# Kernel tuning notes

Measured on AMD Instinct MI355X. Metric: run time of the kernel, lower is better.

The kernel has to match this reference:

```python
import jax, jax.numpy as jnp
import numpy as np

B, T, V = 16, 512, 10000
E, H = 300, 256


def setup_inputs() -> dict:
    key = jax.random.key(0)
    ks = jax.random.split(key, 6)
    return {
        "input": jax.random.normal(ks[0], (B, T, V), dtype=jnp.float32),
        "hidden": jax.random.normal(ks[1], (B, H), dtype=jnp.float32),
        "W_emb": jax.random.normal(ks[2], (E, V), dtype=jnp.float32) * 0.02,
        "W_w": jax.random.normal(ks[3], (H, E), dtype=jnp.float32) * 0.05,
        "W_u": jax.random.normal(ks[4], (H, H), dtype=jnp.float32) * 0.05,
        "W_v": jax.random.normal(ks[5], (V, H), dtype=jnp.float32) * 0.05,
    }


def reference(input, hidden, W_emb, W_w, W_u, W_v):
    # Elman-style cell WITHOUT nonlinearity on the hidden state (matches source):
    #   e = x_t @ W_emb^T ; h = e @ W_w^T + h_prev @ W_u^T ; out = softmax(h @ W_v^T)
    def step(h, x_t):  # x_t: [B, V], h: [B, H]
        e = x_t @ W_emb.T                      # [B, E]
        h_new = e @ W_w.T + h @ W_u.T          # [B, H]
        out = jax.nn.softmax(h_new @ W_v.T, axis=1)  # [B, V]
        return h_new, out

    xs = jnp.swapaxes(input, 0, 1)             # [T, B, V]
    _, outs = jax.lax.scan(step, hidden, xs)   # outs: [T, B, V]
    return jnp.swapaxes(outs, 0, 1)            # [B, T, V]
```

## Files before the change

### kernel.cpp

```cpp
#include <hip/hip_runtime.h>

typedef __bf16 bf16x8 __attribute__((ext_vector_type(8)));
typedef float f32x4 __attribute__((ext_vector_type(4)));
typedef unsigned short u16x8 __attribute__((ext_vector_type(8)));

#define VP 10016

__device__ __forceinline__ unsigned short f2bf(float x){
  unsigned u = __builtin_bit_cast(unsigned, x);
  u += 0x7fffu + ((u>>16)&1u);
  return (unsigned short)(u>>16);
}
__device__ __forceinline__ float bf2f(unsigned short h){
  unsigned u = ((unsigned)h)<<16;
  return __builtin_bit_cast(float, u);
}

__global__ __launch_bounds__(256) void k_wvf(const float* __restrict__ W_v,
                                             unsigned short* __restrict__ Wvf,
                                             const float* __restrict__ W_u,
                                             unsigned short* __restrict__ Wu_bf){
  if(blockIdx.x >= 160){
    int i = (blockIdx.x-160)*256 + threadIdx.x;
    const float4 v = *(const float4*)(W_u + (size_t)i*4);
    unsigned a = (unsigned)f2bf(v.x) | ((unsigned)f2bf(v.y)<<16);
    unsigned b = (unsigned)f2bf(v.z) | ((unsigned)f2bf(v.w)<<16);
    *(uint2*)(Wu_bf + (size_t)i*4) = make_uint2(a,b);
    return;
  }
  const int t = threadIdx.x;
  const int w = t>>6, lane = t&63;
  const int l15 = lane&15, sl = lane>>4;
  const int vg = blockIdx.x*4 + w;
  const int v = vg*16 + l15;
  #pragma unroll
  for(int kk=0;kk<8;kk++){
    u16x8 pk = {0,0,0,0,0,0,0,0};
    if(v < 10000){
      const float* p = W_v + (size_t)v*256 + kk*32 + sl*8;
      float4 v0 = *(const float4*)p;
      float4 v1 = *(const float4*)(p+4);
      pk[0]=f2bf(v0.x); pk[1]=f2bf(v0.y); pk[2]=f2bf(v0.z); pk[3]=f2bf(v0.w);
      pk[4]=f2bf(v1.x); pk[5]=f2bf(v1.y); pk[6]=f2bf(v1.z); pk[7]=f2bf(v1.w);
    }
    *(u16x8*)(Wvf + ((size_t)vg*8 + kk)*512 + lane*8) = pk;
  }
}

__global__ __launch_bounds__(256) void k_m1(const float* __restrict__ W_w,
                                            const float* __restrict__ W_emb,
                                            unsigned short* __restrict__ M1f){
  __shared__ float4 ww4[16][75];
  const int t = threadIdx.x;
  const int ngrp = blockIdx.y;
  const int n0 = ngrp*16;
  for(int i=t; i<16*75; i+=256){
    int n = i/75, c = i - n*75;
    ww4[n][c] = *(const float4*)(W_w + (size_t)(n0+n)*300 + c*4);
  }
  __syncthreads();
  const int v0 = blockIdx.x*512 + t*2;
  if(v0 >= VP) return;
  const int c  = v0>>5;
  const int sl = (v0>>3)&3;
  const int j  = v0&7;
  unsigned short* outp = M1f + (size_t)(ngrp*313 + c)*512 + sl*128 + j;
  if(v0 >= 10000){
    #pragma unroll
    for(int nn=0;nn<16;nn++) *(unsigned*)&outp[nn*8] = 0u;
    return;
  }
  float acc[16][2];
  #pragma unroll
  for(int nn=0;nn<16;nn++){ acc[nn][0]=0.f; acc[nn][1]=0.f; }
  #pragma unroll 2
  for(int cc=0;cc<75;cc++){
    const float* eb = W_emb + (size_t)(4*cc)*10000 + v0;
    float2 wv0 = *(const float2*)(eb);
    float2 wv1 = *(const float2*)(eb + 10000);
    float2 wv2 = *(const float2*)(eb + 20000);
    float2 wv3 = *(const float2*)(eb + 30000);
    #pragma unroll
    for(int nn=0;nn<16;nn++){
      float4 w = ww4[nn][cc];
      acc[nn][0] += w.x*wv0.x + w.y*wv1.x + w.z*wv2.x + w.w*wv3.x;
      acc[nn][1] += w.x*wv0.y + w.y*wv1.y + w.z*wv2.y + w.w*wv3.y;
    }
  }
  #pragma unroll
  for(int nn=0;nn<16;nn++){
    unsigned pk = (unsigned)f2bf(acc[nn][0]) | ((unsigned)f2bf(acc[nn][1])<<16);
    *(unsigned*)&outp[nn*8] = pk;
  }
}

__global__ __launch_bounds__(512, 4) void k_gemm_a(const float* __restrict__ x,
    const unsigned short* __restrict__ M1f, float* __restrict__ gp, int nsplit){
  __shared__ unsigned short As[32768];
  char* Ab = (char*)As;
  const int t = threadIdx.x;
  const int w = t>>6, lane = t&63;
  const int l15 = lane&15, sl = lane>>4;
  const int mh = w>>2, nq = w&3;
  const int r0 = blockIdx.x*128;
  const int kh = blockIdx.y;
  const int base = 313/nsplit, rem = 313%nsplit;
  const int c0 = kh*base + (kh<rem ? kh : rem);
  const int c1 = c0 + base + (kh<rem ? 1 : 0);

  const unsigned short* mbp[4];
  #pragma unroll
  for(int nt=0;nt<4;nt++)
    mbp[nt] = M1f + (size_t)(nq*4+nt)*313*512 + lane*8;

  f32x4 acc[4][4] = {};
  for(int cs=c0; cs<c1; cs+=8){
    const int cs_n = (c1-cs) < 8 ? (c1-cs) : 8;
    if(lane*4 < cs_n*32){
      const int kk = cs*32 + lane*4;
      const bool ok = (kk + 4 <= 10000);
      const int unit0 = lane>>1;
      const int half8 = (lane&1)*8;
      const float* xp = x + (size_t)(r0 + w*16)*10000 + kk;
      #pragma unroll
      for(int g=0; g<2; g++){
        float4 rX[8];
        #pragma unroll
        for(int j=0;j<8;j++)
          rX[j] = ok ? *(const float4*)(xp + (size_t)(g*8+j)*10000)
                     : float4{0.f,0.f,0.f,0.f};
        #pragma unroll
        for(int j=0;j<8;j++){
          const int r = w*16 + g*8 + j;
          unsigned lo = (unsigned)f2bf(rX[j].x) | ((unsigned)f2bf(rX[j].y)<<16);
          unsigned hi = (unsigned)f2bf(rX[j].z) | ((unsigned)f2bf(rX[j].w)<<16);
          *(uint2*)(Ab + r*512 + (((lane>>1) ^ (r&7))<<4) + half8) = make_uint2(lo,hi);
        }
      }
      (void)unit0;
    }
    __syncthreads();
    for(int cc=0; cc<cs_n; cc++){
      const int c = cs + cc;
      bf16x8 b[4];
      #pragma unroll
      for(int nt=0;nt<4;nt++)
        b[nt] = *(const bf16x8*)(mbp[nt] + (size_t)c*512);
      bf16x8 a[4];
      #pragma unroll
      for(int mt=0;mt<4;mt++){
        const int r = mh*64 + mt*16 + l15;
        const int p = (cc*4 + sl) ^ (l15&7);
        a[mt] = *(const bf16x8*)(Ab + r*512 + p*16);
      }
      #pragma unroll
      for(int mt=0;mt<4;mt++)
        #pragma unroll
        for(int nt=0;nt<4;nt++)
          acc[mt][nt] = __builtin_amdgcn_mfma_f32_16x16x32_bf16(a[mt], b[nt], acc[mt][nt], 0,0,0);
    }
    __syncthreads();
  }

  float* gout = gp + (size_t)kh*2097152;
  #pragma unroll
  for(int mt=0;mt<4;mt++)
    #pragma unroll
    for(int nt=0;nt<4;nt++)
      #pragma unroll
      for(int i2=0;i2<4;i2++){
        int row = r0 + mh*64 + mt*16 + sl*4 + i2;
        int col = nq*64 + nt*16 + l15;
        gout[(size_t)row*256 + col] = acc[mt][nt][i2];
      }
}

__global__ __launch_bounds__(256) void k_reduce(float* __restrict__ gp, int nsplit){
  size_t i = ((size_t)blockIdx.x*256 + threadIdx.x)*4;
  float4 acc = *(const float4*)(gp + i);
  for(int s=1;s<nsplit;s++){
    const float4 v = *(const float4*)(gp + (size_t)s*2097152 + i);
    acc.x+=v.x; acc.y+=v.y; acc.z+=v.z; acc.w+=v.w;
  }
  *(float4*)(gp + i) = acc;
}

__global__ __launch_bounds__(256) void k_matsq(const float* __restrict__ A,
    const float* __restrict__ B, float* __restrict__ C){
  int i = blockIdx.x, j = threadIdx.x;
  __shared__ float arow[256];
  arow[j] = A[i*256 + j];
  __syncthreads();
  float acc = 0.f;
  for(int k=0;k<256;k++) acc += arow[k]*B[k*256 + j];
  C[i*256 + j] = acc;
}

__global__ __launch_bounds__(256) void k_scan_local(const float* __restrict__ g,
    const unsigned short* __restrict__ Wu, float* __restrict__ u_final){
  __shared__ unsigned short ub[2][16*256];
  const int m = blockIdx.x;
  const int t = threadIdx.x, wave=t>>6, lane=t&63, l15=lane&15, sl=lane>>4;
  for(int i=t;i<2048;i+=256) ((unsigned*)ub[0])[i] = 0u;
  __syncthreads();
  int buf = 0;
  for(int j=0;j<16;j++){
    float gv[4][4];
    #pragma unroll
    for(int nt=0;nt<4;nt++)
      #pragma unroll
      for(int i=0;i<4;i++){
        int b = sl*4 + i;
        int n = wave*64 + nt*16 + l15;
        size_t r = (size_t)b*512 + m*16 + j;
        gv[nt][i] = g[r*256 + n];
      }
    bf16x8 af[8];
    #pragma unroll
    for(int kk=0;kk<8;kk++){
      int slot = kk*4 + sl;
      af[kk] = *(const bf16x8*)&ub[buf][l15*256 + ((slot ^ (l15&7))<<3)];
    }
    f32x4 acc[4] = {};
    #pragma unroll
    for(int kk=0;kk<8;kk++)
      #pragma unroll
      for(int nt=0;nt<4;nt++){
        int n = wave*64 + nt*16 + l15;
        bf16x8 bv = *(const bf16x8*)&Wu[(size_t)n*256 + kk*32 + sl*8];
        acc[nt] = __builtin_amdgcn_mfma_f32_16x16x32_bf16(af[kk], bv, acc[nt], 0,0,0);
      }
    #pragma unroll
    for(int nt=0;nt<4;nt++)
      #pragma unroll
      for(int i=0;i<4;i++){
        int b = sl*4 + i;
        int n = wave*64 + nt*16 + l15;
        float v = acc[nt][i] + gv[nt][i];
        ub[buf^1][b*256 + (((n>>3) ^ (b&7))<<3) + (n&7)] = f2bf(v);
        if(j==15) u_final[m*4096 + b*256 + n] = v;
      }
    __syncthreads();
    buf ^= 1;
  }
}

__global__ __launch_bounds__(1024) void k_chunk_scan(const float* __restrict__ hidden,
    const float* __restrict__ u_final, const float* __restrict__ A16,
    float* __restrict__ h_start){
  const int b = blockIdx.x;
  const int t = threadIdx.x;
  const int n = t & 255, q = t >> 8;
  __shared__ float hc[256];
  __shared__ float part[3][256];
  float a[64];
  const float* ap = A16 + (size_t)n*256 + q*64;
  #pragma unroll
  for(int i=0;i<16;i++){
    float4 v = *(const float4*)(ap + i*4);
    a[i*4]=v.x; a[i*4+1]=v.y; a[i*4+2]=v.z; a[i*4+3]=v.w;
  }
  if(q==0){
    float h = hidden[b*256 + n];
    hc[n] = h;
    h_start[b*256 + n] = h;
  }
  __syncthreads();
  for(int m=1;m<32;m++){
    float acc0=0.f, acc1=0.f;
    #pragma unroll
    for(int i=0;i<64;i+=2){
      acc0 += a[i]  *hc[q*64 + i];
      acc1 += a[i+1]*hc[q*64 + i+1];
    }
    float acc = acc0 + acc1;
    if(q) part[q-1][n] = acc;
    __syncthreads();
    if(q==0){
      float v = acc + part[0][n] + part[1][n] + part[2][n]
              + u_final[(size_t)(m-1)*4096 + b*256 + n];
      hc[n] = v;
      h_start[(size_t)m*4096 + b*256 + n] = v;
    }
    __syncthreads();
  }
}

__global__ __launch_bounds__(256) void k_scan_fix(const float* __restrict__ g,
    const unsigned short* __restrict__ Wu, const float* __restrict__ h_start,
    unsigned short* __restrict__ h_bf){
  __shared__ unsigned short ub[2][16*256];
  const int m = blockIdx.x;
  const int t=threadIdx.x, wave=t>>6, lane=t&63, l15=lane&15, sl=lane>>4;
  for(int u=t; u<512; u+=256){
    int b = u>>5, s = u&31;
    const float* hp = h_start + m*4096 + b*256 + s*8;
    float4 v0 = *(const float4*)hp;
    float4 v1 = *(const float4*)(hp+4);
    u16x8 pk;
    pk[0]=f2bf(v0.x); pk[1]=f2bf(v0.y); pk[2]=f2bf(v0.z); pk[3]=f2bf(v0.w);
    pk[4]=f2bf(v1.x); pk[5]=f2bf(v1.y); pk[6]=f2bf(v1.z); pk[7]=f2bf(v1.w);
    *(u16x8*)&ub[0][b*256 + ((s ^ (b&7))<<3)] = pk;
  }
  __syncthreads();
  int buf = 0;
  for(int j=0;j<16;j++){
    float gv[4][4];
    #pragma unroll
    for(int nt=0;nt<4;nt++)
      #pragma unroll
      for(int i=0;i<4;i++){
        int b = sl*4 + i;
        int n = wave*64 + nt*16 + l15;
        size_t r = (size_t)b*512 + m*16 + j;
        gv[nt][i] = g[r*256 + n];
      }
    bf16x8 af[8];
    #pragma unroll
    for(int kk=0;kk<8;kk++){
      int slot = kk*4 + sl;
      af[kk] = *(const bf16x8*)&ub[buf][l15*256 + ((slot ^ (l15&7))<<3)];
    }
    f32x4 acc[4] = {};
    #pragma unroll
    for(int kk=0;kk<8;kk++)
      #pragma unroll
      for(int nt=0;nt<4;nt++){
        int n = wave*64 + nt*16 + l15;
        bf16x8 bv = *(const bf16x8*)&Wu[(size_t)n*256 + kk*32 + sl*8];
        acc[nt] = __builtin_amdgcn_mfma_f32_16x16x32_bf16(af[kk], bv, acc[nt], 0,0,0);
      }
    #pragma unroll
    for(int nt=0;nt<4;nt++)
      #pragma unroll
      for(int i=0;i<4;i++){
        int b = sl*4 + i;
        int n = wave*64 + nt*16 + l15;
        float v = acc[nt][i] + gv[nt][i];
        unsigned short hb = f2bf(v);
        ub[buf^1][b*256 + (((n>>3) ^ (b&7))<<3) + (n&7)] = hb;
        size_t r = (size_t)b*512 + m*16 + j;
        h_bf[r*256 + n] = hb;
      }
    __syncthreads();
    buf ^= 1;
  }
}

__global__ __launch_bounds__(512, 4) void k_gemm_c(const unsigned short* __restrict__ h_bf,
    const unsigned short* __restrict__ Wvf, char* __restrict__ out){
  const int t = threadIdx.x;
  const int w = t>>6, lane = t&63;
  const int l15 = lane&15, sl = lane>>4;
  const int mh = w>>2, nq = w&3;
  const int vt = blockIdx.x, rg = blockIdx.y;
  const int rbase = rg*128 + mh*64;

  const unsigned short* bp[4];
  #pragma unroll
  for(int nt=0;nt<4;nt++)
    bp[nt] = Wvf + (size_t)(vt*16 + nq*4 + nt)*8*512 + lane*8;

  f32x4 acc[4][4] = {};
  #pragma unroll
  for(int kk=0;kk<8;kk++){
    bf16x8 b[4], a[4];
    #pragma unroll
    for(int nt=0;nt<4;nt++)
      b[nt] = *(const bf16x8*)(bp[nt] + (size_t)kk*512);
    #pragma unroll
    for(int mt=0;mt<4;mt++)
      a[mt] = *(const bf16x8*)&h_bf[(size_t)(rbase + mt*16 + l15)*256 + kk*32 + sl*8];
    #pragma unroll
    for(int mt=0;mt<4;mt++)
      #pragma unroll
      for(int nt=0;nt<4;nt++)
        acc[mt][nt] = __builtin_amdgcn_mfma_f32_16x16x32_bf16(a[mt], b[nt], acc[mt][nt], 0,0,0);
  }
  #pragma unroll
  for(int mt=0;mt<4;mt++)
    #pragma unroll
    for(int nt=0;nt<4;nt++){
      const int v = vt*256 + (nq*4+nt)*16 + l15;
      if(v < 10000){
        #pragma unroll
        for(int i=0;i<4;i++){
          int row = rbase + mt*16 + sl*4 + i;
          *(unsigned short*)(out + (size_t)row*40000 + (size_t)v*2) = f2bf(acc[mt][nt][i]);
        }
      }
    }
}

__global__ __launch_bounds__(256) void k_softmax(char* __restrict__ out){
  const int r = blockIdx.x;
  const int t = threadIdx.x;
  const unsigned short* lg = (const unsigned short*)(out + (size_t)r*40000);
  float vals[40];
  float mx = -3.0e38f;
  #pragma unroll
  for(int j=0;j<5;j++){
    int c = j*256 + t;
    if(c < 1250){
      u16x8 p = *(const u16x8*)(lg + (size_t)c*8);
      #pragma unroll
      for(int q=0;q<8;q++){
        float a = bf2f(p[q]);
        vals[j*8+q] = a;
        mx = fmaxf(mx, a);
      }
    }
  }
  #pragma unroll
  for(int o=32;o>=1;o>>=1) mx = fmaxf(mx, __shfl_xor(mx, o));
  __shared__ float redm[4], reds[4];
  if((t&63)==0) redm[t>>6] = mx;
  __syncthreads();
  mx = fmaxf(fmaxf(redm[0],redm[1]), fmaxf(redm[2],redm[3]));
  float s = 0.f;
  #pragma unroll
  for(int j=0;j<5;j++){
    int c = j*256 + t;
    if(c < 1250){
      #pragma unroll
      for(int q=0;q<8;q++){
        float e = __expf(vals[j*8+q]-mx);
        vals[j*8+q] = e;
        s += e;
      }
    }
  }
  #pragma unroll
  for(int o=32;o>=1;o>>=1) s += __shfl_xor(s, o);
  if((t&63)==0) reds[t>>6] = s;
  __syncthreads();
  s = reds[0]+reds[1]+reds[2]+reds[3];
  float inv = 1.0f/s;
  float* op = (float*)(out + (size_t)r*40000);
  #pragma unroll
  for(int j=0;j<5;j++){
    int c = j*256 + t;
    if(c < 1250){
      float4 s0, s1;
      s0.x=vals[j*8+0]*inv; s0.y=vals[j*8+1]*inv; s0.z=vals[j*8+2]*inv; s0.w=vals[j*8+3]*inv;
      s1.x=vals[j*8+4]*inv; s1.y=vals[j*8+5]*inv; s1.z=vals[j*8+6]*inv; s1.w=vals[j*8+7]*inv;
      *(float4*)(op + (size_t)c*8)     = s0;
      *(float4*)(op + (size_t)c*8 + 4) = s1;
    }
  }
}

extern "C" void kernel_launch(void* const* d_in, const int* in_sizes, int n_in,
                              void* d_out, int out_size, void* d_ws, size_t ws_size,
                              hipStream_t stream){
  const float* x      = (const float*)d_in[0];
  const float* hidden = (const float*)d_in[1];
  const float* W_emb  = (const float*)d_in[2];
  const float* W_w    = (const float*)d_in[3];
  const float* W_u    = (const float*)d_in[4];
  const float* W_v    = (const float*)d_in[5];

  const size_t fixed_bytes = 16269312;
  int nsplit = 2;
  if(ws_size >= (size_t)8*2097152*4 + fixed_bytes) nsplit = 8;
  else if(ws_size >= (size_t)4*2097152*4 + fixed_bytes) nsplit = 4;

  char* w = (char*)d_ws;
  size_t off = (size_t)nsplit * 2097152 * 4;
  float*          gp      = (float*)(w + 0);
  unsigned short* M1f     = (unsigned short*)(w + off);          off += 5128192;
  unsigned short* Wvf     = (unsigned short*)(w + off);          off += 5242880;
  unsigned short* Wu_bf   = (unsigned short*)(w + off);          off += 131072;
  float*          u_final = (float*)(w + off);                   off += 524288;
  float*          h_start = (float*)(w + off);                   off += 524288;
  unsigned short* h_bf    = (unsigned short*)(w + off);          off += 4194304;
  float*          powA    = (float*)(w + off);                   off += 262144;
  float*          powB    = (float*)(w + off);                   off += 262144;

  k_m1<<<dim3(20,16),256,0,stream>>>(W_w, W_emb, M1f);
  k_gemm_a<<<dim3(64,nsplit),512,0,stream>>>(x, M1f, gp, nsplit);
  k_wvf<<<224,256,0,stream>>>(W_v, Wvf, W_u, Wu_bf);
  k_matsq<<<256,256,0,stream>>>(W_u,  W_u,  powA);
  k_matsq<<<256,256,0,stream>>>(powA, powA, powB);
  k_matsq<<<256,256,0,stream>>>(powB, powB, powA);
  k_matsq<<<256,256,0,stream>>>(powA, powA, powB);
  k_reduce<<<2048,256,0,stream>>>(gp, nsplit);
  k_scan_local<<<32,256,0,stream>>>(gp, Wu_bf, u_final);
  k_chunk_scan<<<16,1024,0,stream>>>(hidden, u_final, powB, h_start);
  k_scan_fix<<<32,256,0,stream>>>(gp, Wu_bf, h_start, h_bf);
  k_gemm_c<<<dim3(40,64),512,0,stream>>>(h_bf, Wvf, (char*)d_out);
  k_softmax<<<8192,256,0,stream>>>((char*)d_out);
}
```

Measured before the change: 515.0 us.

## Replace sequential chunk scans with matrix-power convolution using precomputed W_u powers

Result: slower. 673.6 us (+30.8%).

```diff
diff --git a/kernel.cpp b/kernel.cpp
--- a/kernel.cpp
+++ b/kernel.cpp
@@ -119,7 +119,6 @@
     if(lane*4 < cs_n*32){
       const int kk = cs*32 + lane*4;
       const bool ok = (kk + 4 <= 10000);
-      const int unit0 = lane>>1;
       const int half8 = (lane&1)*8;
       const float* xp = x + (size_t)(r0 + w*16)*10000 + kk;
       #pragma unroll
@@ -137,7 +136,6 @@
           *(uint2*)(Ab + r*512 + (((lane>>1) ^ (r&7))<<4) + half8) = make_uint2(lo,hi);
         }
       }
-      (void)unit0;
     }
     __syncthreads();
     for(int cc=0; cc<cs_n; cc++){
@@ -185,64 +183,62 @@
   *(float4*)(gp + i) = acc;
 }
 
-__global__ __launch_bounds__(256) void k_matsq(const float* __restrict__ A,
-    const float* __restrict__ B, float* __restrict__ C){
-  int i = blockIdx.x, j = threadIdx.x;
+__global__ __launch_bounds__(256) void k_pow(const float* __restrict__ Wu,
+    float* __restrict__ Pf, unsigned short* __restrict__ Pb, int s){
+  const int i = blockIdx.y + 1;
+  const float* A = (s==1) ? Wu : Pf + (size_t)(s-2)*65536;
+  const float* B = (i==1) ? Wu : Pf + (size_t)(i-2)*65536;
+  const int r = blockIdx.x, j = threadIdx.x;
   __shared__ float arow[256];
-  arow[j] = A[i*256 + j];
+  arow[j] = A[r*256 + j];
   __syncthreads();
   float acc = 0.f;
   for(int k=0;k<256;k++) acc += arow[k]*B[k*256 + j];
-  C[i*256 + j] = acc;
-}
-
-__global__ __launch_bounds__(256) void k_scan_local(const float* __restrict__ g,
-    const unsigned short* __restrict__ Wu, float* __restrict__ u_final){
-  __shared__ unsigned short ub[2][16*256];
+  const size_t o = (size_t)(s+i-2)*65536 + r*256 + j;
+  Pf[o] = acc;
+  Pb[o] = f2bf(acc);
+}
+
+__device__ __forceinline__ void load_afrag(const float* __restrict__ gs, bf16x8* a){
+  #pragma unroll
+  for(int kk=0;kk<8;kk++){
+    float4 v0 = *(const float4*)(gs + kk*32);
+    float4 v1 = *(const float4*)(gs + kk*32 + 4);
+    u16x8 pk;
+    pk[0]=f2bf(v0.x); pk[1]=f2bf(v0.y); pk[2]=f2bf(v0.z); pk[3]=f2bf(v0.w);
+    pk[4]=f2bf(v1.x); pk[5]=f2bf(v1.y); pk[6]=f2bf(v1.z); pk[7]=f2bf(v1.w);
+    a[kk] = __builtin_bit_cast(bf16x8, pk);
+  }
+}
+
+__global__ __launch_bounds__(256) void k_ufinal(const float* __restrict__ g,
+    const unsigned short* __restrict__ Wu_bf, const unsigned short* __restrict__ Pb,
+    float* __restrict__ u_final){
   const int m = blockIdx.x;
-  const int t = threadIdx.x, wave=t>>6, lane=t&63, l15=lane&15, sl=lane>>4;
-  for(int i=t;i<2048;i+=256) ((unsigned*)ub[0])[i] = 0u;
-  __syncthreads();
-  int buf = 0;
-  for(int j=0;j<16;j++){
-    float gv[4][4];
-    #pragma unroll
-    for(int nt=0;nt<4;nt++)
-      #pragma unroll
-      for(int i=0;i<4;i++){
-        int b = sl*4 + i;
-        int n = wave*64 + nt*16 + l15;
-        size_t r = (size_t)b*512 + m*16 + j;
-        gv[nt][i] = g[r*256 + n];
-      }
-    bf16x8 af[8];
-    #pragma unroll
-    for(int kk=0;kk<8;kk++){
-      int slot = kk*4 + sl;
-      af[kk] = *(const bf16x8*)&ub[buf][l15*256 + ((slot ^ (l15&7))<<3)];
-    }
-    f32x4 acc[4] = {};
+  const int t = threadIdx.x, w = t>>6, lane = t&63, l15 = lane&15, sl = lane>>4;
+  f32x4 acc[4] = {};
+  for(int k=0;k<15;k++){
+    bf16x8 a[8];
+    load_afrag(g + ((size_t)l15*512 + m*16 + k)*256 + sl*8, a);
+    const int p = 15-k;
+    const unsigned short* Up = (p==1) ? Wu_bf : Pb + (size_t)(p-2)*65536;
     #pragma unroll
     for(int kk=0;kk<8;kk++)
       #pragma unroll
       for(int nt=0;nt<4;nt++){
-        int n = wave*64 + nt*16 + l15;
-        bf16x8 bv = *(const bf16x8*)&Wu[(size_t)n*256 + kk*32 + sl*8];
-        acc[nt] = __builtin_amdgcn_mfma_f32_16x16x32_bf16(af[kk], bv, acc[nt], 0,0,0);
-      }
-    #pragma unroll
-    for(int nt=0;nt<4;nt++)
-      #pragma unroll
-      for(int i=0;i<4;i++){
-        int b = sl*4 + i;
-        int n = wave*64 + nt*16 + l15;
-        float v = acc[nt][i] + gv[nt][i];
-        ub[buf^1][b*256 + (((n>>3) ^ (b&7))<<3) + (n&7)] = f2bf(v);
-        if(j==15) u_final[m*4096 + b*256 + n] = v;
-      }
-    __syncthreads();
-    buf ^= 1;
-  }
+        const int n = w*64 + nt*16 + l15;
+        bf16x8 bv = *(const bf16x8*)&Up[(size_t)n*256 + kk*32 + sl*8];
+        acc[nt] = __builtin_amdgcn_mfma_f32_16x16x32_bf16(a[kk], bv, acc[nt], 0,0,0);
+      }
+  }
+  #pragma unroll
+  for(int nt=0;nt<4;nt++)
+    #pragma unroll
+    for(int i=0;i<4;i++){
+      const int b = sl*4 + i, n = w*64 + nt*16 + l15;
+      float v = acc[nt][i] + g[((size_t)b*512 + m*16 + 15)*256 + n];
+      u_final[(size_t)m*4096 + b*256 + n] = v;
+    }
 }
 
 __global__ __launch_bounds__(1024) void k_chunk_scan(const float* __restrict__ hidden,
@@ -286,65 +282,51 @@
   }
 }
 
-__global__ __launch_bounds__(256) void k_scan_fix(const float* __restrict__ g,
-    const unsigned short* __restrict__ Wu, const float* __restrict__ h_start,
-    unsigned short* __restrict__ h_bf){
-  __shared__ unsigned short ub[2][16*256];
+__global__ __launch_bounds__(256) void k_hconv(const float* __restrict__ g,
+    const unsigned short* __restrict__ Wu_bf, const unsigned short* __restrict__ Pb,
+    const float* __restrict__ h_start, unsigned short* __restrict__ h_bf){
   const int m = blockIdx.x;
-  const int t=threadIdx.x, wave=t>>6, lane=t&63, l15=lane&15, sl=lane>>4;
-  for(int u=t; u<512; u+=256){
-    int b = u>>5, s = u&31;
-    const float* hp = h_start + m*4096 + b*256 + s*8;
-    float4 v0 = *(const float4*)hp;
-    float4 v1 = *(const float4*)(hp+4);
-    u16x8 pk;
-    pk[0]=f2bf(v0.x); pk[1]=f2bf(v0.y); pk[2]=f2bf(v0.z); pk[3]=f2bf(v0.w);
-    pk[4]=f2bf(v1.x); pk[5]=f2bf(v1.y); pk[6]=f2bf(v1.z); pk[7]=f2bf(v1.w);
-    *(u16x8*)&ub[0][b*256 + ((s ^ (b&7))<<3)] = pk;
-  }
-  __syncthreads();
-  int buf = 0;
-  for(int j=0;j<16;j++){
-    float gv[4][4];
-    #pragma unroll
-    for(int nt=0;nt<4;nt++)
-      #pragma unroll
-      for(int i=0;i<4;i++){
-        int b = sl*4 + i;
-        int n = wave*64 + nt*16 + l15;
-        size_t r = (size_t)b*512 + m*16 + j;
-        gv[nt][i] = g[r*256 + n];
-      }
-    bf16x8 af[8];
-    #pragma unroll
-    for(int kk=0;kk<8;kk++){
-      int slot = kk*4 + sl;
-      af[kk] = *(const bf16x8*)&ub[buf][l15*256 + ((slot ^ (l15&7))<<3)];
-    }
-    f32x4 acc[4] = {};
+  const int y = blockIdx.y;
+  const int j = (y<8) ? y : 23-y;
+  const int t = threadIdx.x, w = t>>6, lane = t&63, l15 = lane&15, sl = lane>>4;
+  f32x4 acc[4] = {};
+  for(int tt=0;tt<j;tt++){
+    bf16x8 a[8];
+    load_afrag(g + ((size_t)l15*512 + m*16 + tt)*256 + sl*8, a);
+    const int p = j-tt;
+    const unsigned short* Up = (p==1) ? Wu_bf : Pb + (size_t)(p-2)*65536;
     #pragma unroll
     for(int kk=0;kk<8;kk++)
       #pragma unroll
       for(int nt=0;nt<4;nt++){
-        int n = wave*64 + nt*16 + l15;
-        bf16x8 bv = *(const bf16x8*)&Wu[(size_t)n*256 + kk*32 + sl*8];
-        acc[nt] = __builtin_amdgcn_mfma_f32_16x16x32_bf16(af[kk], bv, acc[nt], 0,0,0);
-      }
-    #pragma unroll
-    for(int nt=0;nt<4;nt++)
-      #pragma unroll
-      for(int i=0;i<4;i++){
-        int b = sl*4 + i;
-        int n = wave*64 + nt*16 + l15;
-        float v = acc[nt][i] + gv[nt][i];
-        unsigned short hb = f2bf(v);
-        ub[buf^1][b*256 + (((n>>3) ^ (b&7))<<3) + (n&7)] = hb;
-        size_t r = (size_t)b*512 + m*16 + j;
-        h_bf[r*256 + n] = hb;
-      }
-    __syncthreads();
-    buf ^= 1;
-  }
+        const int n = w*64 + nt*16 + l15;
+        bf16x8 bv = *(const bf16x8*)&Up[(size_t)n*256 + kk*32 + sl*8];
+        acc[nt] = __builtin_amdgcn_mfma_f32_16x16x32_bf16(a[kk], bv, acc[nt], 0,0,0);
+      }
+  }
+  {
+    bf16x8 a[8];
+    load_afrag(h_start + (size_t)m*4096 + l15*256 + sl*8, a);
+    const int p = j+1;
+    const unsigned short* Up = (p==1) ? Wu_bf : Pb + (size_t)(p-2)*65536;
+    #pragma unroll
+    for(int kk=0;kk<8;kk++)
+      #pragma unroll
+      for(int nt=0;nt<4;nt++){
+        const int n = w*64 + nt*16 + l15;
+        bf16x8 bv = *(const bf16x8*)&Up[(size_t)n*256 + kk*32 + sl*8];
+        acc[nt] = __builtin_amdgcn_mfma_f32_16x16x32_bf16(a[kk], bv, acc[nt], 0,0,0);
+      }
+  }
+  #pragma unroll
+  for(int nt=0;nt<4;nt++)
+    #pragma unroll
+    for(int i=0;i<4;i++){
+      const int b = sl*4 + i, n = w*64 + nt*16 + l15;
+      const size_t r = (size_t)b*512 + m*16 + j;
+      float v = acc[nt][i] + g[r*256 + n];
+      h_bf[r*256 + n] = f2bf(v);
+    }
 }
 
 __global__ __launch_bounds__(512, 4) void k_gemm_c(const unsigned short* __restrict__ h_bf,
@@ -474,20 +456,21 @@
   float*          u_final = (float*)(w + off);                   off += 524288;
   float*          h_start = (float*)(w + off);                   off += 524288;
   unsigned short* h_bf    = (unsigned short*)(w + off);          off += 4194304;
-  float*          powA    = (float*)(w + off);                   off += 262144;
-  float*          powB    = (float*)(w + off);                   off += 262144;
+
+  float*          Pf = gp + 2097152;
+  unsigned short* Pb = (unsigned short*)(Pf + 15*65536);
 
   k_m1<<<dim3(20,16),256,0,stream>>>(W_w, W_emb, M1f);
   k_gemm_a<<<dim3(64,nsplit),512,0,stream>>>(x, M1f, gp, nsplit);
   k_wvf<<<224,256,0,stream>>>(W_v, Wvf, W_u, Wu_bf);
-  k_matsq<<<256,256,0,stream>>>(W_u,  W_u,  powA);
-  k_matsq<<<256,256,0,stream>>>(powA, powA, powB);
-  k_matsq<<<256,256,0,stream>>>(powB, powB, powA);
-  k_matsq<<<256,256,0,stream>>>(powA, powA, powB);
   k_reduce<<<2048,256,0,stream>>>(gp, nsplit);
-  k_scan_local<<<32,256,0,stream>>>(gp, Wu_bf, u_final);
-  k_chunk_scan<<<16,1024,0,stream>>>(hidden, u_final, powB, h_start);
-  k_scan_fix<<<32,256,0,stream>>>(gp, Wu_bf, h_start, h_bf);
+  k_pow<<<dim3(256,1),256,0,stream>>>(W_u, Pf, Pb, 1);
+  k_pow<<<dim3(256,2),256,0,stream>>>(W_u, Pf, Pb, 2);
+  k_pow<<<dim3(256,4),256,0,stream>>>(W_u, Pf, Pb, 4);
+  k_pow<<<dim3(256,8),256,0,stream>>>(W_u, Pf, Pb, 8);
+  k_ufinal<<<32,256,0,stream>>>(gp, Wu_bf, Pb, u_final);
+  k_chunk_scan<<<16,1024,0,stream>>>(hidden, u_final, Pf + 14*65536, h_start);
+  k_hconv<<<dim3(32,16),256,0,stream>>>(gp, Wu_bf, Pb, h_start, h_bf);
   k_gemm_c<<<dim3(40,64),512,0,stream>>>(h_bf, Wvf, (char*)d_out);
   k_softmax<<<8192,256,0,stream>>>((char*)d_out);
 }
```
